# Optimization experiments

Measured on AMD Instinct MI355X. Metric: run time of the kernel, lower is better.

The kernel has to match this reference:

```python
import jax, jax.numpy as jnp
import numpy as np

PE_DIM = 64

def _layernorm(x, g, b, eps=1e-5):
    m = jnp.mean(x, -1, keepdims=True)
    v = jnp.mean((x - m) ** 2, -1, keepdims=True)
    return (x - m) * jax.lax.rsqrt(v + eps) * g + b

def _sinusoidal_pe(t, dim=PE_DIM):
    half = dim // 2
    freqs = jnp.exp(-jnp.log(10000.0) * jnp.arange(half) / half).astype(t.dtype)
    ang = t[..., None] * freqs  # [..., half]
    return jnp.concatenate([jnp.sin(ang), jnp.cos(ang)], -1)

def _bilinear(feats, b, t, x, y):
    # feats [B,Wl,H,W,D]; b,t int32 [B,Q,Wl,M] (b broadcastable); x,y in [0,1]
    # matches torch grid_sample(mode=bilinear, padding_mode=border, align_corners=False)
    H, W = feats.shape[2], feats.shape[3]
    px = x * W - 0.5
    py = y * H - 0.5
    x0 = jnp.floor(px); y0 = jnp.floor(py)
    wx = (px - x0)[..., None]; wy = (py - y0)[..., None]
    x0i = jnp.clip(x0.astype(jnp.int32), 0, W - 1)
    x1i = jnp.clip(x0.astype(jnp.int32) + 1, 0, W - 1)
    y0i = jnp.clip(y0.astype(jnp.int32), 0, H - 1)
    y1i = jnp.clip(y0.astype(jnp.int32) + 1, 0, H - 1)
    v00 = feats[b, t, y0i, x0i]  # [B,Q,Wl,M,D]
    v01 = feats[b, t, y0i, x1i]
    v10 = feats[b, t, y1i, x0i]
    v11 = feats[b, t, y1i, x1i]
    return (v00 * (1 - wy) * (1 - wx) + v01 * (1 - wy) * wx
            + v10 * wy * (1 - wx) + v11 * wy * wx)

def setup_inputs() -> dict:
    key = jax.random.key(0)
    ks = jax.random.split(key, 20)
    B, Q, Wl, H, W, D, M = 4, 300, 8, 64, 64, 256, 4
    s = 0.02
    inp = {
        'q': jax.random.normal(ks[0], (B, Q, D), jnp.float32),
        'kv_feats': jax.random.normal(ks[1], (B, Wl, H, W, D), jnp.float32),
        'kv_mask': jnp.zeros((B, Wl, H, W), jnp.bool_),
        'delta_sec': jax.random.normal(ks[2], (B, Q, Wl), jnp.float32),
        'w_ref': jax.random.normal(ks[3], (D, 2), jnp.float32) * s,
        'b_ref': jnp.zeros((2,), jnp.float32),
        'w_delta': jax.random.normal(ks[4], (2 * D, 3 * M), jnp.float32) * s,
        'b_delta': jnp.zeros((3 * M,), jnp.float32),
        'w_alpha': jax.random.normal(ks[5], (2 * D, M), jnp.float32) * s,
        'b_alpha': jnp.zeros((M,), jnp.float32),
        'lam': jnp.array(1.0, jnp.float32),
        'w_proj': jax.random.normal(ks[6], (D, D), jnp.float32) * s,
        'b_proj': jnp.zeros((D,), jnp.float32),
        'ln1_g': jnp.ones((D,), jnp.float32), 'ln1_b': jnp.zeros((D,), jnp.float32),
        'ln2_g': jnp.ones((D,), jnp.float32), 'ln2_b': jnp.zeros((D,), jnp.float32),
        'w_ffn1': jax.random.normal(ks[7], (D, 4 * D), jnp.float32) * s,
        'b_ffn1': jnp.zeros((4 * D,), jnp.float32),
        'w_ffn2': jax.random.normal(ks[8], (4 * D, D), jnp.float32) * s,
        'b_ffn2': jnp.zeros((D,), jnp.float32),
        'w_rel': jax.random.normal(ks[9], (PE_DIM, D), jnp.float32) * s,
        'b_rel': jnp.zeros((D,), jnp.float32),
    }
    return inp

def reference(q, kv_feats, kv_mask, delta_sec, w_ref, b_ref, w_delta, b_delta,
              w_alpha, b_alpha, lam, w_proj, b_proj, ln1_g, ln1_b, ln2_g, ln2_b,
              w_ffn1, b_ffn1, w_ffn2, b_ffn2, w_rel, b_rel):
    B, Q, D = q.shape
    Wl = kv_feats.shape[1]
    M = w_alpha.shape[1]

    qn = _layernorm(q, ln1_g, ln1_b)
    rel_feat = _sinusoidal_pe(delta_sec) @ w_rel + b_rel          # [B,Q,Wl,D]
    psi = jnp.concatenate([jnp.broadcast_to(qn[:, :, None, :], (B, Q, Wl, D)),
                           rel_feat], -1)                          # [B,Q,Wl,2D]

    delta = (psi @ w_delta + b_delta).reshape(B, Q, Wl, M, 3)
    logits = psi @ w_alpha + b_alpha                               # [B,Q,Wl,M]
    ref = jax.nn.sigmoid(qn @ w_ref + b_ref)                       # [B,Q,2]
    coords = ref[:, :, None, None, :] + jnp.tanh(delta[..., :2])   # [B,Q,Wl,M,2]
    coords = jnp.clip(coords, 0.0, 1.0)
    delta_t = jnp.tanh(delta[..., 2])                              # [B,Q,Wl,M]

    # mask features (mask==True -> invalid -> zero)
    feats = kv_feats * (~kv_mask)[..., None].astype(kv_feats.dtype)

    # temporal trilinear indices
    base = jnp.arange(Wl, dtype=q.dtype).reshape(1, 1, Wl, 1)
    target = base + delta_t
    t0f = jnp.clip(jnp.floor(target), 0, Wl - 1)
    t1f = jnp.clip(t0f + 1, 0, Wl - 1)
    alpha = (target - t0f)[..., None]
    t0 = t0f.astype(jnp.int32); t1 = t1f.astype(jnp.int32)

    bidx = jnp.arange(B, dtype=jnp.int32).reshape(B, 1, 1, 1)
    cx = coords[..., 0]; cy = coords[..., 1]
    s0 = _bilinear(feats, bidx, t0, cx, cy)                        # [B,Q,Wl,M,D]
    s1 = _bilinear(feats, bidx, t1, cx, cy)
    sampled = s0 * (1 - alpha) + s1 * alpha

    lam_sp = jax.nn.softplus(lam)
    weights = jax.nn.softmax(logits - lam_sp * jnp.abs(delta_sec)[..., None], axis=-1)
    agg = jnp.sum(weights[..., None] * sampled, axis=(2, 3))       # [B,Q,D]

    out = q + (agg @ w_proj + b_proj)
    h = _layernorm(out, ln2_g, ln2_b)
    ffn = jax.nn.gelu(h @ w_ffn1 + b_ffn1, approximate=False) @ w_ffn2 + b_ffn2
    return out + ffn
```

## Files before the change

### kernel.cpp

```cpp
#include <hip/hip_runtime.h>
#include <math.h>

#define Bn 4
#define Qn 300
#define WL 8
#define Hh 64
#define Ww 64
#define Dd 256
#define Mm 4

__device__ __forceinline__ float wave_reduce(float v) {
#pragma unroll
    for (int off = 32; off > 0; off >>= 1) v += __shfl_down(v, off, 64);
    return v;
}

using h2_t = _Float16 __attribute__((ext_vector_type(2)));

__device__ __forceinline__ unsigned packh2(float a, float b) {
    auto h = __builtin_amdgcn_cvt_pkrtz(a, b);
    union { decltype(h) h; unsigned u; } x; x.h = h; return x.u;
}

__device__ __forceinline__ h2_t u2h2(unsigned u) {
    union { unsigned u; h2_t h; } x; x.u = u; return x.h;
}

__device__ __forceinline__ float dot2p(unsigned a, unsigned w, float acc) {
#if __has_builtin(__builtin_amdgcn_fdot2)
    return __builtin_amdgcn_fdot2(u2h2(a), u2h2(w), acc, false);
#else
    h2_t A = u2h2(a), W = u2h2(w);
    return acc + (float)A.x * (float)W.x + (float)A.y * (float)W.y;
#endif
}

__device__ __forceinline__ float dot8h(uint4 av, uint4 wv, float acc) {
    acc = dot2p(av.x, wv.x, acc);
    acc = dot2p(av.y, wv.y, acc);
    acc = dot2p(av.z, wv.z, acc);
    acc = dot2p(av.w, wv.w, acc);
    return acc;
}

__global__ void __launch_bounds__(512, 4) k_front(const float* __restrict__ wp,
                                                  const float* __restrict__ wf1,
                                                  const float* __restrict__ wf2,
                                                  unsigned* __restrict__ pk,
                                                  const float* __restrict__ q,
                                                  const float* __restrict__ g1,
                                                  const float* __restrict__ b1,
                                                  const float* __restrict__ w_ref,
                                                  const float* __restrict__ b_ref,
                                                  const float* __restrict__ dsec,
                                                  const float* __restrict__ w_rel,
                                                  const float* __restrict__ b_rel,
                                                  const float* __restrict__ w_delta,
                                                  const float* __restrict__ b_delta,
                                                  const float* __restrict__ w_alpha,
                                                  const float* __restrict__ b_alpha,
                                                  const unsigned char* __restrict__ mask,
                                                  const float* __restrict__ feats,
                                                  float* __restrict__ agg) {
    int bid = blockIdx.x, t = threadIdx.x;

    if (bid < 576) {
        int i = bid * 512 + t;
        if (i < 32768) {
            int p = i & 3, c = (i >> 2) & 255, g = i >> 10;
            pk[i] = packh2(wp[(g * 8 + 2 * p) * 256 + c], wp[(g * 8 + 2 * p + 1) * 256 + c]);
        } else if (i < 163840) {
            int i2 = i - 32768;
            int p = i2 & 3, c = (i2 >> 2) & 1023, g = i2 >> 12;
            pk[i] = packh2(wf1[(g * 8 + 2 * p) * 1024 + c], wf1[(g * 8 + 2 * p + 1) * 1024 + c]);
        } else {
            int i3 = i - 163840;
            int p = i3 & 3, c = (i3 >> 2) & 255, g = i3 >> 10;
            pk[i] = packh2(wf2[(g * 8 + 2 * p) * 256 + c], wf2[(g * 8 + 2 * p + 1) * 256 + c]);
        }
        return;
    }

    __shared__ float sqn[256];
    __shared__ float pe[8][64];
    __shared__ float rel[8][260];
    __shared__ __align__(16) float WcT[16 * 516];
    __shared__ float res[8][16];
    __shared__ float red[32];
    unsigned* Prec = (unsigned*)&pe[0][0];

    int bq = bid - 576;
    int ch = t & 255;
    bool lo = t < 256;
    int lane = t & 63, wv = t >> 6;

    float wr[64];
#pragma unroll
    for (int k = 0; k < 64; k++) wr[k] = w_rel[k * Dd + ch];

    for (int u = t; u < 512 * 16; u += 512) {
        int k = u >> 4, jj = u & 15;
        float w = (jj < 12) ? w_delta[k * 12 + jj] : w_alpha[k * 4 + (jj - 12)];
        WcT[jj * 516 + k] = w;
    }

    float x = lo ? q[bq * Dd + ch] : 0.f;
    {
        float sx = x, sxx = x * x;
#pragma unroll
        for (int off = 32; off > 0; off >>= 1) {
            sx += __shfl_down(sx, off, 64);
            sxx += __shfl_down(sxx, off, 64);
        }
        if (lane == 0) { red[wv] = sx; red[8 + wv] = sxx; }
    }

    if (lo) {
        int wl = t >> 5, i2 = t & 31;
        float f = expf(-logf(10000.f) * (float)i2 * (1.f / 32.f));
        float a = dsec[bq * WL + wl] * f;
        pe[wl][i2] = sinf(a);
        pe[wl][i2 + 32] = cosf(a);
    }
    __syncthreads();

    float m  = (red[0] + red[1] + red[2] + red[3]) * (1.f / Dd);
    float ms = (red[8] + red[9] + red[10] + red[11]) * (1.f / Dd);
    float vvar = ms - m * m;
    float y = 0.f;
    if (lo) { y = (x - m) * rsqrtf(vvar + 1e-5f) * g1[ch] + b1[ch]; sqn[ch] = y; }

    {
        float c0 = lo ? y * w_ref[2 * ch] : 0.f;
        float c1 = lo ? y * w_ref[2 * ch + 1] : 0.f;
#pragma unroll
        for (int off = 32; off > 0; off >>= 1) {
            c0 += __shfl_down(c0, off, 64);
            c1 += __shfl_down(c1, off, 64);
        }
        if (lane == 0) { red[16 + wv] = c0; red[24 + wv] = c1; }
    }
    __syncthreads();

    float ref0, ref1;
    {
        float s0 = red[16] + red[17] + red[18] + red[19] + b_ref[0];
        float s1 = red[24] + red[25] + red[26] + red[27] + b_ref[1];
        ref0 = 1.f / (1.f + expf(-s0));
        ref1 = 1.f / (1.f + expf(-s1));
    }
    {
        float brl = b_rel[ch];
        int wh = t >> 8;
#pragma unroll
        for (int w2 = 0; w2 < 4; w2++) {
            int wl = wh * 4 + w2;
            const float4* p4 = (const float4*)&pe[wl][0];
            float r = brl;
#pragma unroll
            for (int k4 = 0; k4 < 16; k4++) {
                float4 p = p4[k4];
                r += p.x * wr[4 * k4] + p.y * wr[4 * k4 + 1]
                   + p.z * wr[4 * k4 + 2] + p.w * wr[4 * k4 + 3];
            }
            rel[wl][ch] = r;
        }
    }
    __syncthreads();

    int j = wv;
    {
        int jj = lane >> 2, kq = lane & 3;
        const float4* wrow = (const float4*)&WcT[jj * 516 + kq * 128];
        const float4* arow = (kq < 2) ? (const float4*)&sqn[kq * 128]
                                      : (const float4*)&rel[j][(kq - 2) * 128];
        float s = 0.f;
#pragma unroll 8
        for (int k4 = 0; k4 < 32; k4++) {
            float4 a = arow[k4], w = wrow[k4];
            s += a.x * w.x + a.y * w.y + a.z * w.z + a.w * w.w;
        }
        s += __shfl_xor(s, 1, 64);
        s += __shfl_xor(s, 2, 64);
        if ((lane & 3) == 0) {
            float b = (jj < 12) ? b_delta[jj] : b_alpha[jj - 12];
            res[j][jj] = s + b;
        }

        if (lane < 4) {
            int mm = lane;
            float l0 = res[j][12], l1 = res[j][13], l2 = res[j][14], l3 = res[j][15];
            float mx = fmaxf(fmaxf(l0, l1), fmaxf(l2, l3));
            float inv = 1.f / (expf(l0 - mx) + expf(l1 - mx) + expf(l2 - mx) + expf(l3 - mx));
            float wgt = expf(res[j][12 + mm] - mx) * inv;

            float cx = fminf(fmaxf(ref0 + tanhf(res[j][mm * 3 + 0]), 0.f), 1.f);
            float cy = fminf(fmaxf(ref1 + tanhf(res[j][mm * 3 + 1]), 0.f), 1.f);
            float tgt = (float)j + tanhf(res[j][mm * 3 + 2]);
            float t0f = fminf(fmaxf(floorf(tgt), 0.f), (float)(WL - 1));
            float t1f = fminf(t0f + 1.f, (float)(WL - 1));
            float alpha = tgt - t0f;
            float px = cx * (float)Ww - 0.5f, py = cy * (float)Hh - 0.5f;
            float fx = floorf(px), fy = floorf(py);
            float wx = px - fx, wy = py - fy;
            int X0 = (int)fminf(fmaxf(fx, 0.f), (float)(Ww - 1));
            int X1 = (int)fminf(fmaxf(fx + 1.f, 0.f), (float)(Ww - 1));
            int Y0 = (int)fminf(fmaxf(fy, 0.f), (float)(Hh - 1));
            int Y1 = (int)fminf(fmaxf(fy + 1.f, 0.f), (float)(Hh - 1));
            int T0 = (int)t0f, T1 = (int)t1f;

            float w00 = (1.f - wy) * (1.f - wx), w01 = (1.f - wy) * wx;
            float w10 = wy * (1.f - wx), w11 = wy * wx;
            float wt0 = wgt * (1.f - alpha), wt1 = wgt * alpha;

            int b = bq / Qn;
            int base0 = (b * WL + T0) * Hh;
            int base1 = (b * WL + T1) * Hh;
            int i00 = (base0 + Y0) * Ww + X0, i01 = (base0 + Y0) * Ww + X1;
            int i10 = (base0 + Y1) * Ww + X0, i11 = (base0 + Y1) * Ww + X1;
            int j00 = (base1 + Y0) * Ww + X0, j01 = (base1 + Y0) * Ww + X1;
            int j10 = (base1 + Y1) * Ww + X0, j11 = (base1 + Y1) * Ww + X1;

            unsigned* rec = &Prec[(j * 4 + mm) * 16];
            rec[0] = __float_as_uint(wt0 * w00 * (mask[i00] ? 0.f : 1.f));
            rec[1] = __float_as_uint(wt0 * w01 * (mask[i01] ? 0.f : 1.f));
            rec[2] = __float_as_uint(wt0 * w10 * (mask[i10] ? 0.f : 1.f));
            rec[3] = __float_as_uint(wt0 * w11 * (mask[i11] ? 0.f : 1.f));
            rec[4] = __float_as_uint(wt1 * w00 * (mask[j00] ? 0.f : 1.f));
            rec[5] = __float_as_uint(wt1 * w01 * (mask[j01] ? 0.f : 1.f));
            rec[6] = __float_as_uint(wt1 * w10 * (mask[j10] ? 0.f : 1.f));
            rec[7] = __float_as_uint(wt1 * w11 * (mask[j11] ? 0.f : 1.f));
            rec[8] = i00; rec[9] = i01; rec[10] = i10; rec[11] = i11;
            rec[12] = j00; rec[13] = j01; rec[14] = j10; rec[15] = j11;
        }

        const float4* f4 = (const float4*)feats;
        float4 acc = {0.f, 0.f, 0.f, 0.f};
#pragma unroll
        for (int p = 0; p < 4; p++) {
            const unsigned* rec = &Prec[(j * 4 + p) * 16];
#pragma unroll
            for (int cn = 0; cn < 8; cn++) {
                float w = __uint_as_float(rec[cn]);
                size_t idx = rec[8 + cn];
                float4 vv = f4[idx * 64 + lane];
                acc.x += w * vv.x; acc.y += w * vv.y; acc.z += w * vv.z; acc.w += w * vv.w;
            }
        }
        ((float4*)&rel[j][0])[lane] = acc;
    }
    __syncthreads();

    if (t < 256) {
        agg[(size_t)bq * Dd + t] = rel[0][t] + rel[1][t] + rel[2][t] + rel[3][t]
                                 + rel[4][t] + rel[5][t] + rel[6][t] + rel[7][t];
    }
}

template<int R>
__device__ __forceinline__ void out_body(int row0,
        const float* __restrict__ q, const float* __restrict__ agg,
        const unsigned* __restrict__ pkP, const float* __restrict__ b_proj,
        const float* __restrict__ g2, const float* __restrict__ b2,
        const unsigned* __restrict__ pkF1, const float* __restrict__ b_ffn1,
        const unsigned* __restrict__ pkF2, const float* __restrict__ b_ffn2,
        float* __restrict__ out,
        unsigned* sA2, float* sO, unsigned* sH2, unsigned* sF2, float* sX, float* sRed) {
    int t = threadIdx.x;
    int j8 = t >> 7, c7 = t & 127;

    for (int u = t; u < 128 * R; u += 1024) {
        int r = u >> 7, c2 = u & 127;
        float2 av = *(const float2*)&agg[(size_t)(row0 + r) * Dd + 2 * c2];
        sA2[r * 128 + c2] = packh2(av.x, av.y);
    }
    __syncthreads();

    {
        float a0[R], a1[R];
#pragma unroll
        for (int r = 0; r < R; r++) { a0[r] = 0.f; a1[r] = 0.f; }
#pragma unroll
        for (int gg = 0; gg < 4; gg++) {
            int g = j8 * 4 + gg;
            uint4 wv0 = *(const uint4*)&pkP[((unsigned)(g * 256 + c7)) * 4];
            uint4 wv1 = *(const uint4*)&pkP[((unsigned)(g * 256 + c7 + 128)) * 4];
#pragma unroll
            for (int r = 0; r < R; r++) {
                uint4 av = ((const uint4*)&sA2[r * 128])[g];
                a0[r] = dot8h(av, wv0, a0[r]);
                a1[r] = dot8h(av, wv1, a1[r]);
            }
        }
#pragma unroll
        for (int r = 0; r < R; r++) {
            sX[(j8 * R + r) * 256 + c7] = a0[r];
            sX[(j8 * R + r) * 256 + c7 + 128] = a1[r];
        }
    }
    __syncthreads();

    for (int u = t; u < 256 * R; u += 1024) {
        int r = u >> 8, cc = u & 255;
        float o = q[(size_t)(row0 + r) * Dd + cc] + b_proj[cc];
#pragma unroll
        for (int jj = 0; jj < 8; jj++) o += sX[(jj * R + r) * 256 + cc];
        sO[r * 256 + cc] = o;
    }
    __syncthreads();

    {
        int wv = t >> 6, l = t & 63;
        if (wv < R) {
            float4 vv = ((const float4*)&sO[wv * 256])[l];
            float s = vv.x + vv.y + vv.z + vv.w;
            s = __shfl(wave_reduce(s), 0, 64);
            float mean = s * (1.f / 256.f);
            float d0 = vv.x - mean, d1 = vv.y - mean, d2 = vv.z - mean, d3 = vv.w - mean;
            float ss = d0 * d0 + d1 * d1 + d2 * d2 + d3 * d3;
            ss = __shfl(wave_reduce(ss), 0, 64);
            float rstd = rsqrtf(ss * (1.f / 256.f) + 1e-5f);
            if (l == 0) { sRed[wv * 2] = mean; sRed[wv * 2 + 1] = rstd; }
        }
    }
    __syncthreads();
    for (int u = t; u < 128 * R; u += 1024) {
        int r = u >> 7, c2 = u & 127;
        int cc = 2 * c2;
        float mean = sRed[r * 2], rstd = sRed[r * 2 + 1];
        float h0 = (sO[r * 256 + cc] - mean) * rstd * g2[cc] + b2[cc];
        float h1 = (sO[r * 256 + cc + 1] - mean) * rstd * g2[cc + 1] + b2[cc + 1];
        sH2[r * 128 + c2] = packh2(h0, h1);
    }
    __syncthreads();

    {
        int h = t >> 9, c2c = t & 511;
        float f0[R], f1[R];
#pragma unroll
        for (int r = 0; r < R; r++) { f0[r] = 0.f; f1[r] = 0.f; }
#pragma unroll 2
        for (int gg = 0; gg < 16; gg++) {
            int g = h * 16 + gg;
            uint4 wv0 = *(const uint4*)&pkF1[((unsigned)(g * 1024 + c2c)) * 4];
            uint4 wv1 = *(const uint4*)&pkF1[((unsigned)(g * 1024 + c2c + 512)) * 4];
#pragma unroll
            for (int r = 0; r < R; r++) {
                uint4 av = ((const uint4*)&sH2[r * 128])[g];
                f0[r] = dot8h(av, wv0, f0[r]);
                f1[r] = dot8h(av, wv1, f1[r]);
            }
        }
        float* dst = sX + h * (R * 1024);
#pragma unroll
        for (int r = 0; r < R; r++) {
            dst[r * 1024 + c2c] = f0[r];
            dst[r * 1024 + c2c + 512] = f1[r];
        }
    }
    __syncthreads();

    for (int u = t; u < 512 * R; u += 1024) {
        int r = u >> 9, p = u & 511;
        float2 pa = ((const float2*)&sX[r * 1024])[p];
        float2 pb = ((const float2*)&sX[R * 1024 + r * 1024])[p];
        float2 bf = *(const float2*)&b_ffn1[2 * p];
        float x0 = pa.x + pb.x + bf.x;
        float x1 = pa.y + pb.y + bf.y;
        float e0 = 0.5f * x0 * (1.f + erff(x0 * 0.70710678118654752f));
        float e1 = 0.5f * x1 * (1.f + erff(x1 * 0.70710678118654752f));
        sF2[r * 512 + p] = packh2(e0, e1);
    }
    __syncthreads();

    {
        float a0[R], a1[R];
#pragma unroll
        for (int r = 0; r < R; r++) { a0[r] = 0.f; a1[r] = 0.f; }
#pragma unroll 2
        for (int gg = 0; gg < 16; gg++) {
            int g = j8 * 16 + gg;
            uint4 wv0 = *(const uint4*)&pkF2[((unsigned)(g * 256 + c7)) * 4];
            uint4 wv1 = *(const uint4*)&pkF2[((unsigned)(g * 256 + c7 + 128)) * 4];
#pragma unroll
            for (int r = 0; r < R; r++) {
                uint4 av = ((const uint4*)&sF2[r * 512])[g];
                a0[r] = dot8h(av, wv0, a0[r]);
                a1[r] = dot8h(av, wv1, a1[r]);
            }
        }
#pragma unroll
        for (int r = 0; r < R; r++) {
            sX[(j8 * R + r) * 256 + c7] = a0[r];
            sX[(j8 * R + r) * 256 + c7 + 128] = a1[r];
        }
    }
    __syncthreads();

    for (int u = t; u < 256 * R; u += 1024) {
        int r = u >> 8, cc = u & 255;
        float s = b_ffn2[cc];
#pragma unroll
        for (int jj = 0; jj < 8; jj++) s += sX[(jj * R + r) * 256 + cc];
        out[(size_t)(row0 + r) * Dd + cc] = sO[r * 256 + cc] + s;
    }
}

__global__ void __launch_bounds__(1024) k_out(const float* __restrict__ q,
                                              const float* __restrict__ agg,
                                              const unsigned* __restrict__ pkP,
                                              const float* __restrict__ b_proj,
                                              const float* __restrict__ g2,
                                              const float* __restrict__ b2,
                                              const unsigned* __restrict__ pkF1,
                                              const float* __restrict__ b_ffn1,
                                              const unsigned* __restrict__ pkF2,
                                              const float* __restrict__ b_ffn2,
                                              float* __restrict__ out) {
    __shared__ __align__(16) unsigned sA2[5 * 128];
    __shared__ __align__(16) float sO[5 * 256];
    __shared__ __align__(16) unsigned sH2[5 * 128];
    __shared__ __align__(16) unsigned sF2[5 * 512];
    __shared__ __align__(16) float sX[10240];
    __shared__ float sRed[16];
    __shared__ float pad[5120];
    if (b_ffn2 == nullptr) pad[threadIdx.x & 1023] = 0.f;

    int bid = blockIdx.x;
    if (bid < 176) {
        out_body<5>(bid * 5, q, agg, pkP, b_proj, g2, b2, pkF1, b_ffn1, pkF2, b_ffn2,
                    out, sA2, sO, sH2, sF2, sX, sRed);
    } else {
        out_body<4>(880 + (bid - 176) * 4, q, agg, pkP, b_proj, g2, b2, pkF1, b_ffn1,
                    pkF2, b_ffn2, out, sA2, sO, sH2, sF2, sX, sRed);
    }
}

extern "C" void kernel_launch(void* const* d_in, const int* in_sizes, int n_in,
                              void* d_out, int out_size, void* d_ws, size_t ws_size,
                              hipStream_t stream) {
    const float* q        = (const float*)d_in[0];
    const float* kv_feats = (const float*)d_in[1];
    const unsigned char* kv_mask = (const unsigned char*)d_in[2];
    const float* delta_sec= (const float*)d_in[3];
    const float* w_ref    = (const float*)d_in[4];
    const float* b_ref    = (const float*)d_in[5];
    const float* w_delta  = (const float*)d_in[6];
    const float* b_delta  = (const float*)d_in[7];
    const float* w_alpha  = (const float*)d_in[8];
    const float* b_alpha  = (const float*)d_in[9];
    const float* w_proj   = (const float*)d_in[11];
    const float* b_proj   = (const float*)d_in[12];
    const float* ln1_g    = (const float*)d_in[13];
    const float* ln1_b    = (const float*)d_in[14];
    const float* ln2_g    = (const float*)d_in[15];
    const float* ln2_b    = (const float*)d_in[16];
    const float* w_ffn1   = (const float*)d_in[17];
    const float* b_ffn1   = (const float*)d_in[18];
    const float* w_ffn2   = (const float*)d_in[19];
    const float* b_ffn2   = (const float*)d_in[20];
    const float* w_rel    = (const float*)d_in[21];
    const float* b_rel    = (const float*)d_in[22];
    float* out = (float*)d_out;

    unsigned* pk   = (unsigned*)d_ws;
    unsigned* pkP  = pk;
    unsigned* pkF1 = pk + 32768;
    unsigned* pkF2 = pk + 163840;
    float*    agg  = (float*)(pk + 294912);

    const int BQ = Bn * Qn;
    k_front<<<dim3(576 + BQ), dim3(512), 0, stream>>>(w_proj, w_ffn1, w_ffn2, pk,
                                                      q, ln1_g, ln1_b, w_ref, b_ref,
                                                      delta_sec, w_rel, b_rel,
                                                      w_delta, b_delta, w_alpha, b_alpha,
                                                      kv_mask, kv_feats, agg);
    k_out<<<dim3(256), dim3(1024), 0, stream>>>(q, agg, pkP, b_proj, ln2_g, ln2_b,
                                                pkF1, b_ffn1, pkF2, b_ffn2, out);
}
```

Baseline: 279.8 us.

## Restructure output MLP kernel to 512-thread blocks with fewer rows each

Each k_out block now uses 512 threads and handles 3 or 2 rows instead of 5 or 4, and the grid grows from 256 to 480 blocks. The per-thread work split changes to match: 4 K-slices for the projection and FFN2, and 4 output columns per thread in FFN1. The shared-memory padding that limited occupancy is removed and launch bounds request 6 blocks per CU. This spreads the output MLP over more CUs with higher occupancy, at the cost of less weight reuse per block, since each block rereads the full packed weights for fewer rows.

Result: no change. 281.6 us (+0.6%).

```diff
diff --git a/kernel.cpp b/kernel.cpp
--- a/kernel.cpp
+++ b/kernel.cpp
@@ -267,9 +267,9 @@
         float* __restrict__ out,
         unsigned* sA2, float* sO, unsigned* sH2, unsigned* sF2, float* sX, float* sRed) {
     int t = threadIdx.x;
-    int j8 = t >> 7, c7 = t & 127;
-
-    for (int u = t; u < 128 * R; u += 1024) {
+    int j4 = t >> 7, c7 = t & 127;
+
+    for (int u = t; u < 128 * R; u += 512) {
         int r = u >> 7, c2 = u & 127;
         float2 av = *(const float2*)&agg[(size_t)(row0 + r) * Dd + 2 * c2];
         sA2[r * 128 + c2] = packh2(av.x, av.y);
@@ -280,9 +280,9 @@
         float a0[R], a1[R];
 #pragma unroll
         for (int r = 0; r < R; r++) { a0[r] = 0.f; a1[r] = 0.f; }
-#pragma unroll
-        for (int gg = 0; gg < 4; gg++) {
-            int g = j8 * 4 + gg;
+#pragma unroll 2
+        for (int gg = 0; gg < 8; gg++) {
+            int g = j4 * 8 + gg;
             uint4 wv0 = *(const uint4*)&pkP[((unsigned)(g * 256 + c7)) * 4];
             uint4 wv1 = *(const uint4*)&pkP[((unsigned)(g * 256 + c7 + 128)) * 4];
 #pragma unroll
@@ -294,17 +294,17 @@
         }
 #pragma unroll
         for (int r = 0; r < R; r++) {
-            sX[(j8 * R + r) * 256 + c7] = a0[r];
-            sX[(j8 * R + r) * 256 + c7 + 128] = a1[r];
-        }
-    }
-    __syncthreads();
-
-    for (int u = t; u < 256 * R; u += 1024) {
+            sX[(j4 * R + r) * 256 + c7] = a0[r];
+            sX[(j4 * R + r) * 256 + c7 + 128] = a1[r];
+        }
+    }
+    __syncthreads();
+
+    for (int u = t; u < 256 * R; u += 512) {
         int r = u >> 8, cc = u & 255;
         float o = q[(size_t)(row0 + r) * Dd + cc] + b_proj[cc];
 #pragma unroll
-        for (int jj = 0; jj < 8; jj++) o += sX[(jj * R + r) * 256 + cc];
+        for (int jj = 0; jj < 4; jj++) o += sX[(jj * R + r) * 256 + cc];
         sO[r * 256 + cc] = o;
     }
     __syncthreads();
@@ -324,7 +324,7 @@
         }
     }
     __syncthreads();
-    for (int u = t; u < 128 * R; u += 1024) {
+    for (int u = t; u < 128 * R; u += 512) {
         int r = u >> 7, c2 = u & 127;
         int cc = 2 * c2;
         float mean = sRed[r * 2], rstd = sRed[r * 2 + 1];
@@ -335,32 +335,37 @@
     __syncthreads();
 
     {
-        int h = t >> 9, c2c = t & 511;
-        float f0[R], f1[R];
-#pragma unroll
-        for (int r = 0; r < R; r++) { f0[r] = 0.f; f1[r] = 0.f; }
-#pragma unroll 2
+        int h = t >> 8, c8 = t & 255;
+        float f0[R], f1[R], f2[R], f3[R];
+#pragma unroll
+        for (int r = 0; r < R; r++) { f0[r] = 0.f; f1[r] = 0.f; f2[r] = 0.f; f3[r] = 0.f; }
         for (int gg = 0; gg < 16; gg++) {
             int g = h * 16 + gg;
-            uint4 wv0 = *(const uint4*)&pkF1[((unsigned)(g * 1024 + c2c)) * 4];
-            uint4 wv1 = *(const uint4*)&pkF1[((unsigned)(g * 1024 + c2c + 512)) * 4];
+            uint4 w0 = *(const uint4*)&pkF1[((unsigned)(g * 1024 + c8)) * 4];
+            uint4 w1 = *(const uint4*)&pkF1[((unsigned)(g * 1024 + c8 + 256)) * 4];
+            uint4 w2 = *(const uint4*)&pkF1[((unsigned)(g * 1024 + c8 + 512)) * 4];
+            uint4 w3 = *(const uint4*)&pkF1[((unsigned)(g * 1024 + c8 + 768)) * 4];
 #pragma unroll
             for (int r = 0; r < R; r++) {
                 uint4 av = ((const uint4*)&sH2[r * 128])[g];
-                f0[r] = dot8h(av, wv0, f0[r]);
-                f1[r] = dot8h(av, wv1, f1[r]);
+                f0[r] = dot8h(av, w0, f0[r]);
+                f1[r] = dot8h(av, w1, f1[r]);
+                f2[r] = dot8h(av, w2, f2[r]);
+                f3[r] = dot8h(av, w3, f3[r]);
             }
         }
         float* dst = sX + h * (R * 1024);
 #pragma unroll
         for (int r = 0; r < R; r++) {
-            dst[r * 1024 + c2c] = f0[r];
-            dst[r * 1024 + c2c + 512] = f1[r];
-        }
-    }
-    __syncthreads();
-
-    for (int u = t; u < 512 * R; u += 1024) {
+            dst[r * 1024 + c8]       = f0[r];
+            dst[r * 1024 + c8 + 256] = f1[r];
+            dst[r * 1024 + c8 + 512] = f2[r];
+            dst[r * 1024 + c8 + 768] = f3[r];
+        }
+    }
+    __syncthreads();
+
+    for (int u = t; u < 512 * R; u += 512) {
         int r = u >> 9, p = u & 511;
         float2 pa = ((const float2*)&sX[r * 1024])[p];
         float2 pb = ((const float2*)&sX[R * 1024 + r * 1024])[p];
@@ -378,8 +383,8 @@
 #pragma unroll
         for (int r = 0; r < R; r++) { a0[r] = 0.f; a1[r] = 0.f; }
 #pragma unroll 2
-        for (int gg = 0; gg < 16; gg++) {
-            int g = j8 * 16 + gg;
+        for (int gg = 0; gg < 32; gg++) {
+            int g = j4 * 32 + gg;
             uint4 wv0 = *(const uint4*)&pkF2[((unsigned)(g * 256 + c7)) * 4];
             uint4 wv1 = *(const uint4*)&pkF2[((unsigned)(g * 256 + c7 + 128)) * 4];
 #pragma unroll
@@ -391,47 +396,45 @@
         }
 #pragma unroll
         for (int r = 0; r < R; r++) {
-            sX[(j8 * R + r) * 256 + c7] = a0[r];
-            sX[(j8 * R + r) * 256 + c7 + 128] = a1[r];
-        }
-    }
-    __syncthreads();
-
-    for (int u = t; u < 256 * R; u += 1024) {
+            sX[(j4 * R + r) * 256 + c7] = a0[r];
+            sX[(j4 * R + r) * 256 + c7 + 128] = a1[r];
+        }
+    }
+    __syncthreads();
+
+    for (int u = t; u < 256 * R; u += 512) {
         int r = u >> 8, cc = u & 255;
         float s = b_ffn2[cc];
 #pragma unroll
-        for (int jj = 0; jj < 8; jj++) s += sX[(jj * R + r) * 256 + cc];
+        for (int jj = 0; jj < 4; jj++) s += sX[(jj * R + r) * 256 + cc];
         out[(size_t)(row0 + r) * Dd + cc] = sO[r * 256 + cc] + s;
     }
 }
 
-__global__ void __launch_bounds__(1024) k_out(const float* __restrict__ q,
-                                              const float* __restrict__ agg,
-                                              const unsigned* __restrict__ pkP,
-                                              const float* __restrict__ b_proj,
-                                              const float* __restrict__ g2,
-                                              const float* __restrict__ b2,
-                                              const unsigned* __restrict__ pkF1,
-                                              const float* __restrict__ b_ffn1,
-                                              const unsigned* __restrict__ pkF2,
-                                              const float* __restrict__ b_ffn2,
-                                              float* __restrict__ out) {
-    __shared__ __align__(16) unsigned sA2[5 * 128];
-    __shared__ __align__(16) float sO[5 * 256];
-    __shared__ __align__(16) unsigned sH2[5 * 128];
-    __shared__ __align__(16) unsigned sF2[5 * 512];
-    __shared__ __align__(16) float sX[10240];
-    __shared__ float sRed[16];
-    __shared__ float pad[5120];
-    if (b_ffn2 == nullptr) pad[threadIdx.x & 1023] = 0.f;
+__global__ void __launch_bounds__(512, 6) k_out(const float* __restrict__ q,
+                                                const float* __restrict__ agg,
+                                                const unsigned* __restrict__ pkP,
+                                                const float* __restrict__ b_proj,
+                                                const float* __restrict__ g2,
+                                                const float* __restrict__ b2,
+                                                const unsigned* __restrict__ pkF1,
+                                                const float* __restrict__ b_ffn1,
+                                                const unsigned* __restrict__ pkF2,
+                                                const float* __restrict__ b_ffn2,
+                                                float* __restrict__ out) {
+    __shared__ __align__(16) unsigned sA2[3 * 128];
+    __shared__ __align__(16) float sO[3 * 256];
+    __shared__ __align__(16) unsigned sH2[3 * 128];
+    __shared__ __align__(16) unsigned sF2[3 * 512];
+    __shared__ __align__(16) float sX[6144];
+    __shared__ float sRed[8];
 
     int bid = blockIdx.x;
-    if (bid < 176) {
-        out_body<5>(bid * 5, q, agg, pkP, b_proj, g2, b2, pkF1, b_ffn1, pkF2, b_ffn2,
+    if (bid < 240) {
+        out_body<3>(bid * 3, q, agg, pkP, b_proj, g2, b2, pkF1, b_ffn1, pkF2, b_ffn2,
                     out, sA2, sO, sH2, sF2, sX, sRed);
     } else {
-        out_body<4>(880 + (bid - 176) * 4, q, agg, pkP, b_proj, g2, b2, pkF1, b_ffn1,
+        out_body<2>(720 + (bid - 240) * 2, q, agg, pkP, b_proj, g2, b2, pkF1, b_ffn1,
                     pkF2, b_ffn2, out, sA2, sO, sH2, sF2, sX, sRed);
     }
 }
@@ -475,6 +478,6 @@
                                                       delta_sec, w_rel, b_rel,
                                                       w_delta, b_delta, w_alpha, b_alpha,
                                                       kv_mask, kv_feats, agg);
-    k_out<<<dim3(256), dim3(1024), 0, stream>>>(q, agg, pkP, b_proj, ln2_g, ln2_b,
-                                                pkF1, b_ffn1, pkF2, b_ffn2, out);
-}
+    k_out<<<dim3(480), dim3(512), 0, stream>>>(q, agg, pkP, b_proj, ln2_g, ln2_b,
+                                               pkF1, b_ffn1, pkF2, b_ffn2, out);
+}
```

## Pack weights eight-per-thread, store offset-logit weights as fp16, split gather accumulators

Applied to the files above, without the earlier changes.

The weight-packing blocks now have each thread read eight rows and write one uint4 of packed halves, which cuts the packing grid from 576 to 144 blocks. The per-query combined delta/alpha weight matrix is staged in shared memory as packed fp16 pairs instead of fp32. This halves its LDS footprint and the reads in the dot product. The bilinear gather accumulation uses two independent accumulators to shorten the dependency chain. Storing those weights in fp16 slightly lowers the precision of the offset and logit computation.

Result: slower. 287.3 us (+2.7%).

```diff
diff --git a/kernel.cpp b/kernel.cpp
--- a/kernel.cpp
+++ b/kernel.cpp
@@ -64,32 +64,44 @@
                                                   float* __restrict__ agg) {
     int bid = blockIdx.x, t = threadIdx.x;
 
-    if (bid < 576) {
-        int i = bid * 512 + t;
-        if (i < 32768) {
-            int p = i & 3, c = (i >> 2) & 255, g = i >> 10;
-            pk[i] = packh2(wp[(g * 8 + 2 * p) * 256 + c], wp[(g * 8 + 2 * p + 1) * 256 + c]);
-        } else if (i < 163840) {
-            int i2 = i - 32768;
-            int p = i2 & 3, c = (i2 >> 2) & 1023, g = i2 >> 12;
-            pk[i] = packh2(wf1[(g * 8 + 2 * p) * 1024 + c], wf1[(g * 8 + 2 * p + 1) * 1024 + c]);
+    if (bid < 144) {
+        int u = bid * 512 + t;
+        float r[8];
+        unsigned* dst;
+        if (u < 8192) {
+            int g = u >> 8, c = u & 255;
+#pragma unroll
+            for (int k = 0; k < 8; k++) r[k] = wp[(g * 8 + k) * 256 + c];
+            dst = &pk[(unsigned)(g * 256 + c) * 4];
+        } else if (u < 40960) {
+            int u2 = u - 8192;
+            int g = u2 >> 10, c = u2 & 1023;
+#pragma unroll
+            for (int k = 0; k < 8; k++) r[k] = wf1[(g * 8 + k) * 1024 + c];
+            dst = &pk[32768 + (unsigned)(g * 1024 + c) * 4];
         } else {
-            int i3 = i - 163840;
-            int p = i3 & 3, c = (i3 >> 2) & 255, g = i3 >> 10;
-            pk[i] = packh2(wf2[(g * 8 + 2 * p) * 256 + c], wf2[(g * 8 + 2 * p + 1) * 256 + c]);
-        }
+            int u3 = u - 40960;
+            int g = u3 >> 8, c = u3 & 255;
+#pragma unroll
+            for (int k = 0; k < 8; k++) r[k] = wf2[(g * 8 + k) * 256 + c];
+            dst = &pk[163840 + (unsigned)(g * 256 + c) * 4];
+        }
+        uint4 o;
+        o.x = packh2(r[0], r[1]); o.y = packh2(r[2], r[3]);
+        o.z = packh2(r[4], r[5]); o.w = packh2(r[6], r[7]);
+        *(uint4*)dst = o;
         return;
     }
 
     __shared__ float sqn[256];
     __shared__ float pe[8][64];
     __shared__ float rel[8][260];
-    __shared__ __align__(16) float WcT[16 * 516];
+    __shared__ __align__(16) unsigned WcTh[16 * 260];
     __shared__ float res[8][16];
     __shared__ float red[32];
     unsigned* Prec = (unsigned*)&pe[0][0];
 
-    int bq = bid - 576;
+    int bq = bid - 144;
     int ch = t & 255;
     bool lo = t < 256;
     int lane = t & 63, wv = t >> 6;
@@ -98,10 +110,12 @@
 #pragma unroll
     for (int k = 0; k < 64; k++) wr[k] = w_rel[k * Dd + ch];
 
-    for (int u = t; u < 512 * 16; u += 512) {
-        int k = u >> 4, jj = u & 15;
-        float w = (jj < 12) ? w_delta[k * 12 + jj] : w_alpha[k * 4 + (jj - 12)];
-        WcT[jj * 516 + k] = w;
+    for (int u = t; u < 4096; u += 512) {
+        int kp = u & 255, row = u >> 8;
+        int k0 = 2 * kp, k1 = 2 * kp + 1;
+        float w0 = (row < 12) ? w_delta[k0 * 12 + row] : w_alpha[k0 * 4 + (row - 12)];
+        float w1 = (row < 12) ? w_delta[k1 * 12 + row] : w_alpha[k1 * 4 + (row - 12)];
+        WcTh[row * 260 + kp] = packh2(w0, w1);
     }
 
     float x = lo ? q[bq * Dd + ch] : 0.f;
@@ -171,14 +185,19 @@
     int j = wv;
     {
         int jj = lane >> 2, kq = lane & 3;
-        const float4* wrow = (const float4*)&WcT[jj * 516 + kq * 128];
+        const uint4* wrow = (const uint4*)&WcTh[jj * 260 + kq * 64];
         const float4* arow = (kq < 2) ? (const float4*)&sqn[kq * 128]
                                       : (const float4*)&rel[j][(kq - 2) * 128];
         float s = 0.f;
-#pragma unroll 8
-        for (int k4 = 0; k4 < 32; k4++) {
-            float4 a = arow[k4], w = wrow[k4];
-            s += a.x * w.x + a.y * w.y + a.z * w.z + a.w * w.w;
+#pragma unroll
+        for (int i = 0; i < 16; i++) {
+            uint4 wq = wrow[i];
+            float4 a0 = arow[2 * i], a1 = arow[2 * i + 1];
+            h2_t h0 = u2h2(wq.x), h1 = u2h2(wq.y), h2v = u2h2(wq.z), h3 = u2h2(wq.w);
+            s += a0.x * (float)h0.x + a0.y * (float)h0.y
+               + a0.z * (float)h1.x + a0.w * (float)h1.y
+               + a1.x * (float)h2v.x + a1.y * (float)h2v.y
+               + a1.z * (float)h3.x + a1.w * (float)h3.y;
         }
         s += __shfl_xor(s, 1, 64);
         s += __shfl_xor(s, 2, 64);
@@ -235,10 +254,11 @@
         }
 
         const float4* f4 = (const float4*)feats;
-        float4 acc = {0.f, 0.f, 0.f, 0.f};
+        float4 acc0 = {0.f, 0.f, 0.f, 0.f}, acc1 = {0.f, 0.f, 0.f, 0.f};
 #pragma unroll
         for (int p = 0; p < 4; p++) {
             const unsigned* rec = &Prec[(j * 4 + p) * 16];
+            float4& acc = (p < 2) ? acc0 : acc1;
 #pragma unroll
             for (int cn = 0; cn < 8; cn++) {
                 float w = __uint_as_float(rec[cn]);
@@ -247,6 +267,9 @@
                 acc.x += w * vv.x; acc.y += w * vv.y; acc.z += w * vv.z; acc.w += w * vv.w;
             }
         }
+        float4 acc;
+        acc.x = acc0.x + acc1.x; acc.y = acc0.y + acc1.y;
+        acc.z = acc0.z + acc1.z; acc.w = acc0.w + acc1.w;
         ((float4*)&rel[j][0])[lane] = acc;
     }
     __syncthreads();
@@ -470,7 +493,7 @@
     float*    agg  = (float*)(pk + 294912);
 
     const int BQ = Bn * Qn;
-    k_front<<<dim3(576 + BQ), dim3(512), 0, stream>>>(w_proj, w_ffn1, w_ffn2, pk,
+    k_front<<<dim3(144 + BQ), dim3(512), 0, stream>>>(w_proj, w_ffn1, w_ffn2, pk,
                                                       q, ln1_g, ln1_b, w_ref, b_ref,
                                                       delta_sec, w_rel, b_rel,
                                                       w_delta, b_delta, w_alpha, b_alpha,
```
